# Kernel optimization log

Hardware: AMD Instinct MI355X
Metric: run time of the kernel (lower is better)

Reference implementation:

```python
import jax, jax.numpy as jnp
import numpy as np

N = 100000      # particles
E = 1600000     # particle pairs
B = 1024        # jets (batch); max(part_indicator)+1
C_IN = 64
HID = 32
T = 4           # n_terms
MID = 128
OUT = 128
EPS = 1e-5


def setup_inputs() -> dict:
    key = jax.random.key(0)
    ks = jax.random.split(key, 10)
    s = 0.05
    return {
        "part_features": jax.random.normal(ks[0], (N, C_IN), jnp.float32),
        "part_weight": jax.random.uniform(ks[1], (N, 1), jnp.float32),
        "pair_func": jax.random.normal(ks[2], (E, T), jnp.float32),
        "pair_head": jax.random.randint(ks[3], (E, 1), 0, N),
        "pair_tail": jax.random.randint(ks[4], (E, 1), 0, N),
        "part_indicator": jax.random.randint(ks[5], (N, 1), 0, B),
        "W_sc": jax.random.normal(ks[6], (OUT, C_IN), jnp.float32) * s,
        "g1": jnp.ones((C_IN,), jnp.float32), "b1": jnp.zeros((C_IN,), jnp.float32),
        "W1": jax.random.normal(ks[7], (HID, C_IN), jnp.float32) * s,
        "g2": jnp.ones((T * HID,), jnp.float32), "b2": jnp.zeros((T * HID,), jnp.float32),
        "W2": jax.random.normal(ks[8], (MID, T * HID), jnp.float32) * s,
        "g3": jnp.ones((MID,), jnp.float32), "b3": jnp.zeros((MID,), jnp.float32),
        "W3": jax.random.normal(ks[9], (OUT, MID), jnp.float32) * s,
    }


def weighted_bn(x, w, ind, gamma, beta):
    # segment-sum weighted features per jet -> batch stats over jets (training mode)
    jet = jax.ops.segment_sum(x * w, ind, num_segments=B)  # [B, C]
    mean = jet.mean(0)
    var = jet.var(0, ddof=1)  # unbiased, matches torch var(0, unbiased=True)
    return (x - mean) / jnp.sqrt(var + EPS) * gamma + beta


def reference(part_features, part_weight, pair_func, pair_head, pair_tail,
              part_indicator, W_sc, g1, b1, W1, g2, b2, W2, g3, b3, W3):
    ind = part_indicator[:, 0]
    head = pair_head[:, 0]
    tail = pair_tail[:, 0]

    short_cut = part_features @ W_sc.T                       # [N, OUT]

    h = jax.nn.relu(weighted_bn(part_features, part_weight, ind, g1, b1))
    h = h @ W1.T                                             # [N, HID]
    h = h * part_weight

    # gather tail features, expand by polynomial terms, scatter-add to head
    msg = (h[tail][:, :, None] * pair_func[:, None, :T]).reshape(E, HID * T)
    agg = jax.ops.segment_sum(msg, head, num_segments=N)     # [N, HID*T]

    h = jax.nn.relu(weighted_bn(agg, part_weight, ind, g2, b2)) @ W2.T  # [N, MID]
    h = jax.nn.relu(weighted_bn(h, part_weight, ind, g3, b3)) @ W3.T    # [N, OUT]
    return h + short_cut
```

## Files before the change

kernel.cpp:

```cpp
#include <hip/hip_runtime.h>

#define N_NODES 100000
#define N_EDGES 1600000
#define NB      1024
#define EPSF    1e-5f

#define SCHUNK 256
#define SNBLK ((N_NODES + SCHUNK - 1) / SCHUNK)

#define BUK_SH  7
#define NBUK    ((N_NODES + 127) >> 7)
#define EPB     6400
#define NBA     ((N_EDGES + EPB - 1) / EPB)
#define NCB     (NBUK * NBA)
#define SNB2    ((NCB + SCHUNK - 1) / SCHUNK)
#define CAP     3072

typedef float f32x4  __attribute__((ext_vector_type(4)));
typedef short bf16x8 __attribute__((ext_vector_type(8)));

__device__ __forceinline__ float bf2f(unsigned short u) {
    union { unsigned int i; float f; } v; v.i = ((unsigned int)u) << 16; return v.f;
}
__device__ __forceinline__ unsigned short f2bf(float f) {
    union { float ff; unsigned int i; } v; v.ff = f;
    unsigned int r = v.i + 0x7FFFu + ((v.i >> 16) & 1u);
    return (unsigned short)(r >> 16);
}

template<int C>
__global__ __launch_bounds__(256) void stats_kernel(const float* __restrict__ jet,
                                                    const float* __restrict__ g,
                                                    const float* __restrict__ b,
                                                    float* __restrict__ scale,
                                                    float* __restrict__ shift) {
    int c = blockIdx.x;
    int t = threadIdx.x;
    float s = 0.f, s2 = 0.f;
    for (int r = t; r < NB; r += 256) {
        float v = jet[r * C + c];
        s += v; s2 += v * v;
    }
    __shared__ float ls[256], ls2[256];
    ls[t] = s; ls2[t] = s2;
    __syncthreads();
    for (int ofs = 128; ofs > 0; ofs >>= 1) {
        if (t < ofs) { ls[t] += ls[t + ofs]; ls2[t] += ls2[t + ofs]; }
        __syncthreads();
    }
    if (t == 0) {
        float mean = ls[0] / (float)NB;
        float var  = (ls2[0] - (float)NB * mean * mean) / (float)(NB - 1);
        float sc   = g[c] / sqrtf(var + EPSF);
        scale[c] = sc;
        shift[c] = b[c] - mean * sc;
    }
}

__global__ __launch_bounds__(256) void countI_kernel(const int* __restrict__ ind,
                                                     int* __restrict__ cntI) {
    int n = blockIdx.x * 256 + threadIdx.x;
    if (n < N_NODES) atomicAdd(&cntI[ind[n]], 1);
}

__global__ __launch_bounds__(256) void count_head_kernel(const int* __restrict__ head,
                                                         int* __restrict__ cnt) {
    int e = blockIdx.x * 256 + threadIdx.x;
    if (e < N_EDGES) atomicAdd(&cnt[head[e]], 1);
}

__global__ __launch_bounds__(1024) void countCB_kernel(const int* __restrict__ head,
                                                       int* __restrict__ cnt_cb) {
    __shared__ int h[NBUK];
    int tid = threadIdx.x;
    int blk = blockIdx.x;
    for (int i = tid; i < NBUK; i += 1024) h[i] = 0;
    __syncthreads();
    int e0 = blk * EPB;
    for (int k = tid; k < EPB; k += 1024) {
        int e = e0 + k;
        if (e < N_EDGES) atomicAdd(&h[head[e] >> BUK_SH], 1);
    }
    __syncthreads();
    for (int i = tid; i < NBUK; i += 1024) cnt_cb[i * NBA + blk] = h[i];
}

__global__ __launch_bounds__(SCHUNK) void scanA_kernel(const int* __restrict__ cnt,
                                                       int* __restrict__ part, int n) {
    __shared__ int ls[SCHUNK];
    int t = threadIdx.x;
    int i = blockIdx.x * SCHUNK + t;
    ls[t] = (i < n) ? cnt[i] : 0;
    __syncthreads();
    for (int ofs = SCHUNK / 2; ofs > 0; ofs >>= 1) {
        if (t < ofs) ls[t] += ls[t + ofs];
        __syncthreads();
    }
    if (t == 0) part[blockIdx.x] = ls[0];
}

__global__ __launch_bounds__(1024) void scanB_kernel(const int* __restrict__ in,
                                                     int* __restrict__ out,
                                                     int* __restrict__ out2, int n) {
    __shared__ int ls[1024];
    int t = threadIdx.x;
    int v = (t < n) ? in[t] : 0;
    ls[t] = v;
    __syncthreads();
    for (int ofs = 1; ofs < 1024; ofs <<= 1) {
        int u = (t >= ofs) ? ls[t - ofs] : 0;
        __syncthreads();
        ls[t] += u;
        __syncthreads();
    }
    if (t < n) {
        int e = ls[t] - v;
        out[t] = e;
        if (out2) out2[t] = e;
    }
}

__global__ __launch_bounds__(SCHUNK) void scanC_kernel(const int* __restrict__ cnt,
                                                       const int* __restrict__ poff,
                                                       int* __restrict__ base,
                                                       int* __restrict__ cursor, int n) {
    __shared__ int ls[SCHUNK];
    int t = threadIdx.x;
    int i = blockIdx.x * SCHUNK + t;
    int v = (i < n) ? cnt[i] : 0;
    ls[t] = v;
    __syncthreads();
    for (int ofs = 1; ofs < SCHUNK; ofs <<= 1) {
        int u = (t >= ofs) ? ls[t - ofs] : 0;
        __syncthreads();
        ls[t] += u;
        __syncthreads();
    }
    if (i < n) {
        int bse = poff[blockIdx.x] + ls[t] - v;
        base[i] = bse;
        cursor[i] = bse;
    }
}

__global__ __launch_bounds__(1024) void binC16_kernel(const int* __restrict__ head,
                                                      const int* __restrict__ tail,
                                                      const float* __restrict__ pf,
                                                      const int* __restrict__ cbase,
                                                      uint4* __restrict__ hb16) {
    __shared__ int cur[NBUK];
    int tid = threadIdx.x;
    int blk = blockIdx.x;
    for (int i = tid; i < NBUK; i += 1024) cur[i] = cbase[i * NBA + blk];
    __syncthreads();
    int e0 = blk * EPB;
    for (int k = tid; k < EPB; k += 1024) {
        int e = e0 + k;
        if (e < N_EDGES) {
            int hd = head[e];
            int b = hd >> BUK_SH;
            int slot = atomicAdd(&cur[b], 1);
            float4 pv = ((const float4*)pf)[e];
            uint4 rec;
            rec.x = (unsigned)tail[e] | ((unsigned)(hd & 127) << 21);
            rec.y = (unsigned)f2bf(pv.x) | ((unsigned)f2bf(pv.y) << 16);
            rec.z = (unsigned)f2bf(pv.z) | ((unsigned)f2bf(pv.w) << 16);
            rec.w = 0u;
            hb16[slot] = rec;
        }
    }
}

__global__ __launch_bounds__(512) void sortGather_kernel(const int* __restrict__ cbase,
                                                         const uint4* __restrict__ hb16,
                                                         const unsigned short* __restrict__ hs,
                                                         unsigned short* __restrict__ agg) {
    __shared__ int hcnt[128];
    __shared__ int hbase[128];
    __shared__ int hcur[128];
    __shared__ int tail_l[CAP];
    __shared__ unsigned pf_l[2 * CAP];
    int tid = threadIdx.x;
    int b = blockIdx.x;
    int lo = cbase[b * NBA];
    int hi = (b + 1 < NBUK) ? cbase[(b + 1) * NBA] : N_EDGES;
    int cnt = hi - lo;
    if (tid < 128) hcnt[tid] = 0;
    __syncthreads();

    int wv = tid >> 6, lane = tid & 63;
    int i = lane >> 1, half = lane & 1;

    if (cnt <= CAP) {
        uint4 r0, r1, r2, r3, r4, r5;
        int k0 = lo + tid;
        bool v0 = (k0 < hi),            v1 = (k0 + 512 < hi);
        bool v2 = (k0 + 1024 < hi),     v3 = (k0 + 1536 < hi);
        bool v4 = (k0 + 2048 < hi),     v5 = (k0 + 2560 < hi);
        if (v0) r0 = hb16[k0];
        if (v1) r1 = hb16[k0 + 512];
        if (v2) r2 = hb16[k0 + 1024];
        if (v3) r3 = hb16[k0 + 1536];
        if (v4) r4 = hb16[k0 + 2048];
        if (v5) r5 = hb16[k0 + 2560];
        if (v0) atomicAdd(&hcnt[r0.x >> 21], 1);
        if (v1) atomicAdd(&hcnt[r1.x >> 21], 1);
        if (v2) atomicAdd(&hcnt[r2.x >> 21], 1);
        if (v3) atomicAdd(&hcnt[r3.x >> 21], 1);
        if (v4) atomicAdd(&hcnt[r4.x >> 21], 1);
        if (v5) atomicAdd(&hcnt[r5.x >> 21], 1);
        __syncthreads();
        if (tid < 128) hbase[tid] = hcnt[tid];
        __syncthreads();
        for (int ofs = 1; ofs < 128; ofs <<= 1) {
            int v = (tid < 128 && tid >= ofs) ? hbase[tid - ofs] : 0;
            __syncthreads();
            if (tid < 128) hbase[tid] += v;
            __syncthreads();
        }
        if (tid < 128) {
            int bse = hbase[tid] - hcnt[tid];
            hbase[tid] = bse;
            hcur[tid] = bse;
        }
        __syncthreads();
        if (v0) { int s = atomicAdd(&hcur[r0.x >> 21], 1); tail_l[s] = (int)(r0.x & 0xFFFFFu); pf_l[2*s] = r0.y; pf_l[2*s+1] = r0.z; }
        if (v1) { int s = atomicAdd(&hcur[r1.x >> 21], 1); tail_l[s] = (int)(r1.x & 0xFFFFFu); pf_l[2*s] = r1.y; pf_l[2*s+1] = r1.z; }
        if (v2) { int s = atomicAdd(&hcur[r2.x >> 21], 1); tail_l[s] = (int)(r2.x & 0xFFFFFu); pf_l[2*s] = r2.y; pf_l[2*s+1] = r2.z; }
        if (v3) { int s = atomicAdd(&hcur[r3.x >> 21], 1); tail_l[s] = (int)(r3.x & 0xFFFFFu); pf_l[2*s] = r3.y; pf_l[2*s+1] = r3.z; }
        if (v4) { int s = atomicAdd(&hcur[r4.x >> 21], 1); tail_l[s] = (int)(r4.x & 0xFFFFFu); pf_l[2*s] = r4.y; pf_l[2*s+1] = r4.z; }
        if (v5) { int s = atomicAdd(&hcur[r5.x >> 21], 1); tail_l[s] = (int)(r5.x & 0xFFFFFu); pf_l[2*s] = r5.y; pf_l[2*s+1] = r5.z; }
        __syncthreads();
        for (int j = 0; j < 16; j++) {
            int h7 = (wv << 4) + j;
            int n = (b << BUK_SH) + h7;
            if (n >= N_NODES) break;
            int s0 = hbase[h7], c = hcnt[h7];
            float a0 = 0.f, a1 = 0.f;
            int k = 0;
            for (; k + 4 <= c; k += 4) {
                int t0 = tail_l[s0 + k],     t1 = tail_l[s0 + k + 1];
                int t2 = tail_l[s0 + k + 2], t3 = tail_l[s0 + k + 3];
                unsigned u0 = pf_l[2 * (s0 + k) + half];
                unsigned u1 = pf_l[2 * (s0 + k + 1) + half];
                unsigned u2 = pf_l[2 * (s0 + k + 2) + half];
                unsigned u3 = pf_l[2 * (s0 + k + 3) + half];
                float h0 = bf2f(hs[(size_t)t0 * 32 + i]);
                float h1 = bf2f(hs[(size_t)t1 * 32 + i]);
                float h2 = bf2f(hs[(size_t)t2 * 32 + i]);
                float h3 = bf2f(hs[(size_t)t3 * 32 + i]);
                a0 += h0 * bf2f((unsigned short)(u0 & 0xFFFFu));
                a1 += h0 * bf2f((unsigned short)(u0 >> 16));
                a0 += h1 * bf2f((unsigned short)(u1 & 0xFFFFu));
                a1 += h1 * bf2f((unsigned short)(u1 >> 16));
                a0 += h2 * bf2f((unsigned short)(u2 & 0xFFFFu));
                a1 += h2 * bf2f((unsigned short)(u2 >> 16));
                a0 += h3 * bf2f((unsigned short)(u3 & 0xFFFFu));
                a1 += h3 * bf2f((unsigned short)(u3 >> 16));
            }
            for (; k < c; k++) {
                int t0 = tail_l[s0 + k];
                unsigned u0 = pf_l[2 * (s0 + k) + half];
                float h0 = bf2f(hs[(size_t)t0 * 32 + i]);
                a0 += h0 * bf2f((unsigned short)(u0 & 0xFFFFu));
                a1 += h0 * bf2f((unsigned short)(u0 >> 16));
            }
            unsigned pk = (unsigned)f2bf(a0) | ((unsigned)f2bf(a1) << 16);
            ((unsigned*)agg)[(size_t)n * 64 + lane] = pk;
        }
    } else {
        for (int j = 0; j < 16; j++) {
            int h7 = (wv << 4) + j;
            int n = (b << BUK_SH) + h7;
            if (n >= N_NODES) break;
            unsigned my = (unsigned)h7;
            float a0 = 0.f, a1 = 0.f;
            for (int k = lo; k < hi; k++) {
                uint4 rec = hb16[k];
                if ((rec.x >> 21) == my) {
                    unsigned u0 = (half == 0) ? rec.y : rec.z;
                    float h0 = bf2f(hs[(size_t)(rec.x & 0xFFFFFu) * 32 + i]);
                    a0 += h0 * bf2f((unsigned short)(u0 & 0xFFFFu));
                    a1 += h0 * bf2f((unsigned short)(u0 >> 16));
                }
            }
            unsigned pk = (unsigned)f2bf(a0) | ((unsigned)f2bf(a1) << 16);
            ((unsigned*)agg)[(size_t)n * 64 + lane] = pk;
        }
    }
}

__global__ __launch_bounds__(256) void escatterE_kernel(const int* __restrict__ head,
                                                        int* __restrict__ cursor,
                                                        int* __restrict__ eid) {
    int e = blockIdx.x * 256 + threadIdx.x;
    if (e >= N_EDGES) return;
    int slot = atomicAdd(&cursor[head[e]], 1);
    eid[slot] = e;
}

__global__ __launch_bounds__(256) void scatterI_kernel(const int* __restrict__ ind,
                                                       int* __restrict__ cursorI,
                                                       int* __restrict__ order) {
    int n = blockIdx.x * 256 + threadIdx.x;
    if (n < N_NODES) {
        int pos = atomicAdd(&cursorI[ind[n]], 1);
        order[pos] = n;
    }
}

template<int C>
__global__ __launch_bounds__(256) void bucket_jet_kernel(const float* __restrict__ xx,
                                                         const float* __restrict__ w,
                                                         const int* __restrict__ order,
                                                         const int* __restrict__ baseI,
                                                         const int* __restrict__ cntI,
                                                         float* __restrict__ jet) {
    constexpr int G = 256 / C;
    __shared__ float red[256];
    int b = blockIdx.x;
    int g = threadIdx.x / C;
    int c = threadIdx.x % C;
    int s0 = baseI[b], m = cntI[b];
    float s = 0.f;
    for (int k = g; k < m; k += G) {
        int n = order[s0 + k];
        s += xx[(size_t)n * C + c] * w[n];
    }
    red[threadIdx.x] = s;
    __syncthreads();
    for (int half = G / 2; half > 0; half >>= 1) {
        if (g < half) red[g * C + c] += red[(g + half) * C + c];
        __syncthreads();
    }
    if (g == 0) jet[b * C + c] = red[c];
}

__global__ __launch_bounds__(256) void bucket_jet_bf128_kernel(const unsigned short* __restrict__ xx,
                                                               const float* __restrict__ w,
                                                               const int* __restrict__ order,
                                                               const int* __restrict__ baseI,
                                                               const int* __restrict__ cntI,
                                                               float* __restrict__ jet) {
    __shared__ float redA[256], redB[256];
    int b = blockIdx.x;
    int g  = threadIdx.x >> 6;
    int c2 = threadIdx.x & 63;
    int s0 = baseI[b], m = cntI[b];
    float a0 = 0.f, a1 = 0.f;
    for (int k = g; k < m; k += 4) {
        int n = order[s0 + k];
        float wn = w[n];
        unsigned u = ((const unsigned*)xx)[(size_t)n * 64 + c2];
        a0 += bf2f((unsigned short)(u & 0xFFFFu)) * wn;
        a1 += bf2f((unsigned short)(u >> 16)) * wn;
    }
    redA[threadIdx.x] = a0; redB[threadIdx.x] = a1;
    __syncthreads();
    for (int half = 2; half > 0; half >>= 1) {
        if (g < half) {
            redA[g * 64 + c2] += redA[(g + half) * 64 + c2];
            redB[g * 64 + c2] += redB[(g + half) * 64 + c2];
        }
        __syncthreads();
    }
    if (g == 0) {
        jet[b * 128 + 2 * c2]     = redA[c2];
        jet[b * 128 + 2 * c2 + 1] = redB[c2];
    }
}

#define TILE1 64
__global__ __launch_bounds__(256) void fused1_kernel(const float* __restrict__ x,
                                                     const float* __restrict__ w,
                                                     const float* __restrict__ scale,
                                                     const float* __restrict__ shift,
                                                     const float* __restrict__ W1,
                                                     unsigned short* __restrict__ hs) {
    __shared__ __align__(16) unsigned short xnb[TILE1 * 64];
    __shared__ __align__(16) unsigned short w1b[32 * 64];
    int tid = threadIdx.x;
    int n0  = blockIdx.x * TILE1;
    char* xnb_ = (char*)xnb; char* w1b_ = (char*)w1b;

    for (int idx = tid; idx < TILE1 * 8; idx += 256) {
        int r = idx >> 3, c0 = (idx & 7) << 3;
        int n = n0 + r;
        float4 vA = make_float4(0.f, 0.f, 0.f, 0.f), vB = vA;
        if (n < N_NODES) {
            vA = *(const float4*)&x[(size_t)n * 64 + c0];
            vB = *(const float4*)&x[(size_t)n * 64 + c0 + 4];
        }
        float4 scA = *(const float4*)&scale[c0], scB = *(const float4*)&scale[c0 + 4];
        float4 shA = *(const float4*)&shift[c0], shB = *(const float4*)&shift[c0 + 4];
        unsigned short na[8];
        na[0] = f2bf(fmaxf(fmaf(vA.x, scA.x, shA.x), 0.f));
        na[1] = f2bf(fmaxf(fmaf(vA.y, scA.y, shA.y), 0.f));
        na[2] = f2bf(fmaxf(fmaf(vA.z, scA.z, shA.z), 0.f));
        na[3] = f2bf(fmaxf(fmaf(vA.w, scA.w, shA.w), 0.f));
        na[4] = f2bf(fmaxf(fmaf(vB.x, scB.x, shB.x), 0.f));
        na[5] = f2bf(fmaxf(fmaf(vB.y, scB.y, shB.y), 0.f));
        na[6] = f2bf(fmaxf(fmaf(vB.z, scB.z, shB.z), 0.f));
        na[7] = f2bf(fmaxf(fmaf(vB.w, scB.w, shB.w), 0.f));
        int byte = ((r << 7) + ((idx & 7) << 4)) ^ ((r & 7) << 4);
        *(bf16x8*)(xnb_ + byte) = *(bf16x8*)na;
    }
    for (int idx = tid; idx < 32 * 8; idx += 256) {
        int r = idx >> 3, c0 = (idx & 7) << 3;
        float4 vA = *(const float4*)&W1[(size_t)r * 64 + c0];
        float4 vB = *(const float4*)&W1[(size_t)r * 64 + c0 + 4];
        unsigned short ua[8];
        ua[0] = f2bf(vA.x); ua[1] = f2bf(vA.y); ua[2] = f2bf(vA.z); ua[3] = f2bf(vA.w);
        ua[4] = f2bf(vB.x); ua[5] = f2bf(vB.y); ua[6] = f2bf(vB.z); ua[7] = f2bf(vB.w);
        int byte = ((r << 7) + ((idx & 7) << 4)) ^ ((r & 7) << 4);
        *(bf16x8*)(w1b_ + byte) = *(bf16x8*)ua;
    }
    __syncthreads();

    int wv   = tid >> 6;
    int lane = tid & 63;
    int l15  = lane & 15;
    int lhi  = lane >> 4;

    f32x4 acc[2];
    acc[0] = (f32x4){0.f, 0.f, 0.f, 0.f};
    acc[1] = (f32x4){0.f, 0.f, 0.f, 0.f};

#pragma unroll
    for (int ks = 0; ks < 2; ks++) {
        int rA = (wv << 4) + l15;
        int byteA = ((rA << 7) + (ks << 6) + (lhi << 4)) ^ ((rA & 7) << 4);
        bf16x8 a = *(const bf16x8*)(xnb_ + byteA);
#pragma unroll
        for (int cf = 0; cf < 2; cf++) {
            int rB = (cf << 4) + l15;
            int byteB = ((rB << 7) + (ks << 6) + (lhi << 4)) ^ ((rB & 7) << 4);
            bf16x8 b = *(const bf16x8*)(w1b_ + byteB);
            acc[cf] = __builtin_amdgcn_mfma_f32_16x16x32_bf16(a, b, acc[cf], 0, 0, 0);
        }
    }

#pragma unroll
    for (int cf = 0; cf < 2; cf++) {
        int co = (cf << 4) + l15;
#pragma unroll
        for (int j = 0; j < 4; j++) {
            int n = n0 + (wv << 4) + (lhi << 2) + j;
            if (n < N_NODES) hs[(size_t)n * 32 + co] = f2bf(acc[cf][j] * w[n]);
        }
    }
}

__global__ __launch_bounds__(256) void gather2_kernel(const int* __restrict__ base,
                                                      const int* __restrict__ cnt,
                                                      const int* __restrict__ eid,
                                                      const int* __restrict__ tail,
                                                      const float* __restrict__ pf,
                                                      const unsigned short* __restrict__ hs,
                                                      unsigned short* __restrict__ agg) {
    int n = blockIdx.x * 4 + (threadIdx.x >> 6);
    if (n >= N_NODES) return;
    int lane = threadIdx.x & 63;
    int i = lane >> 1;
    int half = lane & 1;
    int s0 = base[n], c = cnt[n];
    float a0 = 0.f, a1 = 0.f;
    for (int k = 0; k < c; k++) {
        int e0 = eid[s0 + k];
        int t0 = tail[e0];
        float2 p0 = *(const float2*)&pf[(size_t)e0 * 4 + half * 2];
        float h0 = bf2f(hs[(size_t)t0 * 32 + i]);
        a0 += h0 * p0.x; a1 += h0 * p0.y;
    }
    unsigned pk = (unsigned)f2bf(a0) | ((unsigned)f2bf(a1) << 16);
    ((unsigned*)agg)[(size_t)n * 64 + lane] = pk;
}

__global__ __launch_bounds__(256) void edge_kernel(const int* __restrict__ head,
                                                   const int* __restrict__ tail,
                                                   const float* __restrict__ pf,
                                                   const unsigned short* __restrict__ hs,
                                                   float* __restrict__ agg) {
    long long tid = (long long)blockIdx.x * 256 + threadIdx.x;
    if (tid >= (long long)N_EDGES * 128) return;
    int e = (int)(tid >> 7);
    int j = (int)(tid & 127);
    int i = j >> 2, t = j & 3;
    float v = bf2f(hs[(size_t)tail[e] * 32 + i]) * pf[(size_t)e * 4 + t];
    atomicAdd(&agg[(size_t)head[e] * 128 + j], v);
}

#define TILE2 64
template<int INBF, int OUTBF>
__global__ __launch_bounds__(256) void fused2_kernel(const void* __restrict__ xin_,
                                                     const float* __restrict__ scale,
                                                     const float* __restrict__ shift,
                                                     const float* __restrict__ W,
                                                     void* __restrict__ yout_) {
    __shared__ __align__(16) unsigned short xnb[TILE2 * 128];
    __shared__ __align__(16) unsigned short wb[128 * 128];
    int tid = threadIdx.x;
    int n0  = blockIdx.x * TILE2;
    char* xbase = (char*)xnb;
    char* wbase = (char*)wb;

    for (int idx = tid; idx < TILE2 * 16; idx += 256) {
        int r = idx >> 4;
        int c0 = (idx & 15) << 3;
        int n = n0 + r;
        float f[8];
        if (n < N_NODES) {
            if (INBF) {
                const unsigned short* xu = (const unsigned short*)xin_;
                uint4 U = *(const uint4*)(xu + (size_t)n * 128 + c0);
                f[0] = bf2f((unsigned short)(U.x & 0xFFFFu)); f[1] = bf2f((unsigned short)(U.x >> 16));
                f[2] = bf2f((unsigned short)(U.y & 0xFFFFu)); f[3] = bf2f((unsigned short)(U.y >> 16));
                f[4] = bf2f((unsigned short)(U.z & 0xFFFFu)); f[5] = bf2f((unsigned short)(U.z >> 16));
                f[6] = bf2f((unsigned short)(U.w & 0xFFFFu)); f[7] = bf2f((unsigned short)(U.w >> 16));
            } else {
                const float* xf = (const float*)xin_;
                float4 vA = *(const float4*)&xf[(size_t)n * 128 + c0];
                float4 vB = *(const float4*)&xf[(size_t)n * 128 + c0 + 4];
                f[0] = vA.x; f[1] = vA.y; f[2] = vA.z; f[3] = vA.w;
                f[4] = vB.x; f[5] = vB.y; f[6] = vB.z; f[7] = vB.w;
            }
        } else {
#pragma unroll
            for (int q = 0; q < 8; q++) f[q] = 0.f;
        }
        unsigned short ua[8];
#pragma unroll
        for (int q = 0; q < 8; q++)
            ua[q] = f2bf(fmaxf(fmaf(f[q], scale[c0 + q], shift[c0 + q]), 0.f));
        int byte = ((r << 8) + ((idx & 15) << 4)) ^ ((r & 7) << 4);
        *(bf16x8*)(xbase + byte) = *(bf16x8*)ua;
    }
    for (int idx = tid; idx < 128 * 16; idx += 256) {
        int r = idx >> 4;
        int c0 = (idx & 15) << 3;
        float4 vA = *(const float4*)&W[(size_t)r * 128 + c0];
        float4 vB = *(const float4*)&W[(size_t)r * 128 + c0 + 4];
        unsigned short ua[8];
        ua[0] = f2bf(vA.x); ua[1] = f2bf(vA.y); ua[2] = f2bf(vA.z); ua[3] = f2bf(vA.w);
        ua[4] = f2bf(vB.x); ua[5] = f2bf(vB.y); ua[6] = f2bf(vB.z); ua[7] = f2bf(vB.w);
        int byte = ((r << 8) + ((idx & 15) << 4)) ^ ((r & 7) << 4);
        *(bf16x8*)(wbase + byte) = *(bf16x8*)ua;
    }
    __syncthreads();

    int wv   = tid >> 6;
    int lane = tid & 63;
    int l15  = lane & 15;
    int lhi  = lane >> 4;

    f32x4 acc[8];
#pragma unroll
    for (int cf = 0; cf < 8; cf++) acc[cf] = (f32x4){0.f, 0.f, 0.f, 0.f};

#pragma unroll
    for (int ks = 0; ks < 4; ks++) {
        int rA = (wv << 4) + l15;
        int byteA = ((rA << 8) + (ks << 6) + (lhi << 4)) ^ ((rA & 7) << 4);
        bf16x8 a = *(const bf16x8*)(xbase + byteA);
#pragma unroll
        for (int cf = 0; cf < 8; cf++) {
            int rB = (cf << 4) + l15;
            int byteB = ((rB << 8) + (ks << 6) + (lhi << 4)) ^ ((rB & 7) << 4);
            bf16x8 b = *(const bf16x8*)(wbase + byteB);
            acc[cf] = __builtin_amdgcn_mfma_f32_16x16x32_bf16(a, b, acc[cf], 0, 0, 0);
        }
    }

#pragma unroll
    for (int cf = 0; cf < 8; cf++) {
        int col = (cf << 4) + l15;
#pragma unroll
        for (int j = 0; j < 4; j++) {
            int n = n0 + (wv << 4) + (lhi << 2) + j;
            if (n < N_NODES) {
                float v = acc[cf][j];
                if (OUTBF) ((unsigned short*)yout_)[(size_t)n * 128 + col] = f2bf(v);
                else       ((float*)yout_)[(size_t)n * 128 + col] = v;
            }
        }
    }
}

template<int INBF>
__global__ __launch_bounds__(256) void fused3_kernel(const void* __restrict__ h2_,
                                                     const float* __restrict__ x,
                                                     const float* __restrict__ scale,
                                                     const float* __restrict__ shift,
                                                     const float* __restrict__ Wsc,
                                                     const float* __restrict__ W3,
                                                     float* __restrict__ out) {
    __shared__ __align__(16) unsigned short xnb[TILE2 * 128];
    __shared__ __align__(16) unsigned short xrb[TILE2 * 64];
    __shared__ __align__(16) unsigned short wb[128 * 128];
    int tid = threadIdx.x;
    int n0  = blockIdx.x * TILE2;
    char* xbase = (char*)xnb;
    char* rbase = (char*)xrb;
    char* wbase = (char*)wb;

    for (int idx = tid; idx < TILE2 * 16; idx += 256) {
        int r = idx >> 4;
        int c0 = (idx & 15) << 3;
        int n = n0 + r;
        float f[8];
        if (n < N_NODES) {
            if (INBF) {
                const unsigned short* xu = (const unsigned short*)h2_;
                uint4 U = *(const uint4*)(xu + (size_t)n * 128 + c0);
                f[0] = bf2f((unsigned short)(U.x & 0xFFFFu)); f[1] = bf2f((unsigned short)(U.x >> 16));
                f[2] = bf2f((unsigned short)(U.y & 0xFFFFu)); f[3] = bf2f((unsigned short)(U.y >> 16));
                f[4] = bf2f((unsigned short)(U.z & 0xFFFFu)); f[5] = bf2f((unsigned short)(U.z >> 16));
                f[6] = bf2f((unsigned short)(U.w & 0xFFFFu)); f[7] = bf2f((unsigned short)(U.w >> 16));
            } else {
                const float* xf = (const float*)h2_;
                float4 vA = *(const float4*)&xf[(size_t)n * 128 + c0];
                float4 vB = *(const float4*)&xf[(size_t)n * 128 + c0 + 4];
                f[0] = vA.x; f[1] = vA.y; f[2] = vA.z; f[3] = vA.w;
                f[4] = vB.x; f[5] = vB.y; f[6] = vB.z; f[7] = vB.w;
            }
        } else {
#pragma unroll
            for (int q = 0; q < 8; q++) f[q] = 0.f;
        }
        unsigned short ua[8];
#pragma unroll
        for (int q = 0; q < 8; q++)
            ua[q] = f2bf(fmaxf(fmaf(f[q], scale[c0 + q], shift[c0 + q]), 0.f));
        int byte = ((r << 8) + ((idx & 15) << 4)) ^ ((r & 7) << 4);
        *(bf16x8*)(xbase + byte) = *(bf16x8*)ua;
    }
    for (int idx = tid; idx < TILE2 * 8; idx += 256) {
        int r = idx >> 3, c0 = (idx & 7) << 3;
        int n = n0 + r;
        float4 vA = make_float4(0.f, 0.f, 0.f, 0.f), vB = vA;
        if (n < N_NODES) {
            vA = *(const float4*)&x[(size_t)n * 64 + c0];
            vB = *(const float4*)&x[(size_t)n * 64 + c0 + 4];
        }
        unsigned short ua[8];
        ua[0] = f2bf(vA.x); ua[1] = f2bf(vA.y); ua[2] = f2bf(vA.z); ua[3] = f2bf(vA.w);
        ua[4] = f2bf(vB.x); ua[5] = f2bf(vB.y); ua[6] = f2bf(vB.z); ua[7] = f2bf(vB.w);
        int byte = ((r << 7) + ((idx & 7) << 4)) ^ ((r & 7) << 4);
        *(bf16x8*)(rbase + byte) = *(bf16x8*)ua;
    }
    for (int idx = tid; idx < 128 * 8; idx += 256) {
        int r = idx >> 3, c0 = (idx & 7) << 3;
        float4 vA = *(const float4*)&Wsc[(size_t)r * 64 + c0];
        float4 vB = *(const float4*)&Wsc[(size_t)r * 64 + c0 + 4];
        unsigned short ua[8];
        ua[0] = f2bf(vA.x); ua[1] = f2bf(vA.y); ua[2] = f2bf(vA.z); ua[3] = f2bf(vA.w);
        ua[4] = f2bf(vB.x); ua[5] = f2bf(vB.y); ua[6] = f2bf(vB.z); ua[7] = f2bf(vB.w);
        int byte = ((r << 7) + ((idx & 7) << 4)) ^ ((r & 7) << 4);
        *(bf16x8*)(wbase + byte) = *(bf16x8*)ua;
    }
    __syncthreads();

    int wv   = tid >> 6;
    int lane = tid & 63;
    int l15  = lane & 15;
    int lhi  = lane >> 4;

    f32x4 acc[8];
#pragma unroll
    for (int cf = 0; cf < 8; cf++) acc[cf] = (f32x4){0.f, 0.f, 0.f, 0.f};

#pragma unroll
    for (int ks = 0; ks < 2; ks++) {
        int rA = (wv << 4) + l15;
        int byteA = ((rA << 7) + (ks << 6) + (lhi << 4)) ^ ((rA & 7) << 4);
        bf16x8 a = *(const bf16x8*)(rbase + byteA);
#pragma unroll
        for (int cf = 0; cf < 8; cf++) {
            int rB = (cf << 4) + l15;
            int byteB = ((rB << 7) + (ks << 6) + (lhi << 4)) ^ ((rB & 7) << 4);
            bf16x8 b = *(const bf16x8*)(wbase + byteB);
            acc[cf] = __builtin_amdgcn_mfma_f32_16x16x32_bf16(a, b, acc[cf], 0, 0, 0);
        }
    }
    __syncthreads();
    for (int idx = tid; idx < 128 * 16; idx += 256) {
        int r = idx >> 4;
        int c0 = (idx & 15) << 3;
        float4 vA = *(const float4*)&W3[(size_t)r * 128 + c0];
        float4 vB = *(const float4*)&W3[(size_t)r * 128 + c0 + 4];
        unsigned short ua[8];
        ua[0] = f2bf(vA.x); ua[1] = f2bf(vA.y); ua[2] = f2bf(vA.z); ua[3] = f2bf(vA.w);
        ua[4] = f2bf(vB.x); ua[5] = f2bf(vB.y); ua[6] = f2bf(vB.z); ua[7] = f2bf(vB.w);
        int byte = ((r << 8) + ((idx & 15) << 4)) ^ ((r & 7) << 4);
        *(bf16x8*)(wbase + byte) = *(bf16x8*)ua;
    }
    __syncthreads();

#pragma unroll
    for (int ks = 0; ks < 4; ks++) {
        int rA = (wv << 4) + l15;
        int byteA = ((rA << 8) + (ks << 6) + (lhi << 4)) ^ ((rA & 7) << 4);
        bf16x8 a = *(const bf16x8*)(xbase + byteA);
#pragma unroll
        for (int cf = 0; cf < 8; cf++) {
            int rB = (cf << 4) + l15;
            int byteB = ((rB << 8) + (ks << 6) + (lhi << 4)) ^ ((rB & 7) << 4);
            bf16x8 b = *(const bf16x8*)(wbase + byteB);
            acc[cf] = __builtin_amdgcn_mfma_f32_16x16x32_bf16(a, b, acc[cf], 0, 0, 0);
        }
    }

#pragma unroll
    for (int cf = 0; cf < 8; cf++) {
        int col = (cf << 4) + l15;
#pragma unroll
        for (int j = 0; j < 4; j++) {
            int n = n0 + (wv << 4) + (lhi << 2) + j;
            if (n < N_NODES) out[(size_t)n * 128 + col] = acc[cf][j];
        }
    }
}

extern "C" void kernel_launch(void* const* d_in, const int* in_sizes, int n_in,
                              void* d_out, int out_size, void* d_ws, size_t ws_size,
                              hipStream_t stream) {
    const float* x    = (const float*)d_in[0];
    const float* w    = (const float*)d_in[1];
    const float* pf   = (const float*)d_in[2];
    const int*   head = (const int*)d_in[3];
    const int*   tail = (const int*)d_in[4];
    const int*   ind  = (const int*)d_in[5];
    const float* Wsc  = (const float*)d_in[6];
    const float* g1   = (const float*)d_in[7];
    const float* b1   = (const float*)d_in[8];
    const float* W1   = (const float*)d_in[9];
    const float* g2   = (const float*)d_in[10];
    const float* b2   = (const float*)d_in[11];
    const float* W2   = (const float*)d_in[12];
    const float* g3   = (const float*)d_in[13];
    const float* b3   = (const float*)d_in[14];
    const float* W3   = (const float*)d_in[15];
    float* out = (float*)d_out;

    char* p = (char*)d_ws;
    unsigned short* hs = (unsigned short*)p;  p += (size_t)N_NODES * 32 * 2;
    char* aggraw = p;                         p += (size_t)N_NODES * 128 * 4;
    unsigned short* agg_bf = (unsigned short*)aggraw;
    float*          agg_f  = (float*)aggraw;
    uint4* hb16 = (uint4*)(aggraw + (size_t)N_NODES * 128 * 2);
    float* jet1 = (float*)p;                  p += 1024 * 64 * 4;
    float* jet2 = (float*)p;                  p += 1024 * 128 * 4;
    float* jet3 = (float*)p;                  p += 1024 * 128 * 4;
    float* sc1 = (float*)p; p += 64 * 4;  float* sh1 = (float*)p; p += 64 * 4;
    float* sc2 = (float*)p; p += 128 * 4; float* sh2 = (float*)p; p += 128 * 4;
    float* sc3 = (float*)p; p += 128 * 4; float* sh3 = (float*)p; p += 128 * 4;
    int* cnt_e    = (int*)p; p += (size_t)N_NODES * 4;
    int* base_e   = (int*)p; p += (size_t)N_NODES * 4;
    int* cursor_e = (int*)p; p += (size_t)N_NODES * 4;
    int* part     = (int*)p; p += 1024 * 4;
    int* cntI     = (int*)p; p += 1024 * 4;
    int* baseI    = (int*)p; p += 1024 * 4;
    int* cursorI  = (int*)p; p += 1024 * 4;
    int* order    = (int*)p; p += (size_t)N_NODES * 4;
    int* eid      = (int*)p; p += (size_t)N_EDGES * 4;
    size_t need_t2 = (size_t)(p - (char*)d_ws);
    int* cnt_cb   = (int*)p; p += (size_t)NCB * 4;
    int* cbase    = (int*)p; p += (size_t)NCB * 4;
    int* ccur     = (int*)p; p += (size_t)NCB * 4;
    size_t need_t1 = (size_t)(p - (char*)d_ws);
    int tier = (ws_size >= need_t1) ? 1 : (ws_size >= need_t2) ? 2 : 3;

    hipMemsetAsync(cntI, 0, 1024 * sizeof(int), stream);
    countI_kernel<<<(N_NODES + 255) / 256, 256, 0, stream>>>(ind, cntI);
    scanB_kernel<<<1, 1024, 0, stream>>>(cntI, baseI, cursorI, 1024);
    scatterI_kernel<<<(N_NODES + 255) / 256, 256, 0, stream>>>(ind, cursorI, order);

    bucket_jet_kernel<64><<<1024, 256, 0, stream>>>(x, w, order, baseI, cntI, jet1);
    stats_kernel<64><<<64, 256, 0, stream>>>(jet1, g1, b1, sc1, sh1);

    fused1_kernel<<<(N_NODES + TILE1 - 1) / TILE1, 256, 0, stream>>>(
        x, w, sc1, sh1, W1, hs);

    if (tier == 1) {
        countCB_kernel<<<NBA, 1024, 0, stream>>>(head, cnt_cb);
        scanA_kernel<<<SNB2, SCHUNK, 0, stream>>>(cnt_cb, part, NCB);
        scanB_kernel<<<1, 1024, 0, stream>>>(part, part, nullptr, SNB2);
        scanC_kernel<<<SNB2, SCHUNK, 0, stream>>>(cnt_cb, part, cbase, ccur, NCB);
        binC16_kernel<<<NBA, 1024, 0, stream>>>(head, tail, pf, cbase, hb16);
        sortGather_kernel<<<NBUK, 512, 0, stream>>>(cbase, hb16, hs, agg_bf);
    } else if (tier == 2) {
        hipMemsetAsync(cnt_e, 0, N_NODES * sizeof(int), stream);
        count_head_kernel<<<(N_EDGES + 255) / 256, 256, 0, stream>>>(head, cnt_e);
        scanA_kernel<<<SNBLK, SCHUNK, 0, stream>>>(cnt_e, part, N_NODES);
        scanB_kernel<<<1, 1024, 0, stream>>>(part, part, nullptr, SNBLK);
        scanC_kernel<<<SNBLK, SCHUNK, 0, stream>>>(cnt_e, part, base_e, cursor_e, N_NODES);
        escatterE_kernel<<<(N_EDGES + 255) / 256, 256, 0, stream>>>(
            head, cursor_e, eid);
        gather2_kernel<<<(N_NODES + 3) / 4, 256, 0, stream>>>(
            base_e, cnt_e, eid, tail, pf, hs, agg_bf);
    }

    if (tier <= 2) {
        bucket_jet_bf128_kernel<<<1024, 256, 0, stream>>>(agg_bf, w, order, baseI, cntI, jet2);
        stats_kernel<128><<<128, 256, 0, stream>>>(jet2, g2, b2, sc2, sh2);
        fused2_kernel<1, 1><<<(N_NODES + TILE2 - 1) / TILE2, 256, 0, stream>>>(
            agg_bf, sc2, sh2, W2, agg_bf);
        bucket_jet_bf128_kernel<<<1024, 256, 0, stream>>>(agg_bf, w, order, baseI, cntI, jet3);
        stats_kernel<128><<<128, 256, 0, stream>>>(jet3, g3, b3, sc3, sh3);
        fused3_kernel<1><<<(N_NODES + TILE2 - 1) / TILE2, 256, 0, stream>>>(
            agg_bf, x, sc3, sh3, Wsc, W3, out);
    } else {
        hipMemsetAsync(agg_f, 0, (size_t)N_NODES * 128 * sizeof(float), stream);
        edge_kernel<<<(int)(((long long)N_EDGES * 128) / 256), 256, 0, stream>>>(
            head, tail, pf, hs, agg_f);
        bucket_jet_kernel<128><<<1024, 256, 0, stream>>>(agg_f, w, order, baseI, cntI, jet2);
        stats_kernel<128><<<128, 256, 0, stream>>>(jet2, g2, b2, sc2, sh2);
        fused2_kernel<0, 0><<<(N_NODES + TILE2 - 1) / TILE2, 256, 0, stream>>>(
            agg_f, sc2, sh2, W2, agg_f);
        bucket_jet_kernel<128><<<1024, 256, 0, stream>>>(agg_f, w, order, baseI, cntI, jet3);
        stats_kernel<128><<<128, 256, 0, stream>>>(jet3, g3, b3, sc3, sh3);
        fused3_kernel<0><<<(N_NODES + TILE2 - 1) / TILE2, 256, 0, stream>>>(
            agg_f, x, sc3, sh3, Wsc, W3, out);
    }

    (void)in_sizes; (void)n_in; (void)out_size;
}
```

Measured before the change: 282.4 us.

## Replace per-chunk bucket scan with global bucket counts and atomic slot reservation

The edge binning no longer writes a bucket-by-chunk count matrix and runs a three-pass scan over it. Each block now adds its bucket counts atomically into a small global array, which a single-block scan turns into bucket offsets. The binning kernel recounts its chunk locally and reserves contiguous ranges with global atomics. This removes two scan launches and the large count matrix, but edge order within a bucket becomes nondeterministic and head indices are read one extra time. The gather loop is also unrolled from 4 to 8 edges to put more independent loads in flight.

New measurement: 291.3 us. 3.2% more time.

```diff
diff --git a/kernel.cpp b/kernel.cpp
--- a/kernel.cpp
+++ b/kernel.cpp
@@ -12,8 +12,6 @@
 #define NBUK    ((N_NODES + 127) >> 7)
 #define EPB     6400
 #define NBA     ((N_EDGES + EPB - 1) / EPB)
-#define NCB     (NBUK * NBA)
-#define SNB2    ((NCB + SCHUNK - 1) / SCHUNK)
 #define CAP     3072
 
 typedef float f32x4  __attribute__((ext_vector_type(4)));
@@ -69,8 +67,8 @@
     if (e < N_EDGES) atomicAdd(&cnt[head[e]], 1);
 }
 
-__global__ __launch_bounds__(1024) void countCB_kernel(const int* __restrict__ head,
-                                                       int* __restrict__ cnt_cb) {
+__global__ __launch_bounds__(1024) void countB2_kernel(const int* __restrict__ head,
+                                                       int* __restrict__ bcnt) {
     __shared__ int h[NBUK];
     int tid = threadIdx.x;
     int blk = blockIdx.x;
@@ -82,7 +80,8 @@
         if (e < N_EDGES) atomicAdd(&h[head[e] >> BUK_SH], 1);
     }
     __syncthreads();
-    for (int i = tid; i < NBUK; i += 1024) cnt_cb[i * NBA + blk] = h[i];
+    for (int i = tid; i < NBUK; i += 1024)
+        if (h[i] > 0) atomicAdd(&bcnt[i], h[i]);
 }
 
 __global__ __launch_bounds__(SCHUNK) void scanA_kernel(const int* __restrict__ cnt,
@@ -143,23 +142,32 @@
     }
 }
 
-__global__ __launch_bounds__(1024) void binC16_kernel(const int* __restrict__ head,
-                                                      const int* __restrict__ tail,
-                                                      const float* __restrict__ pf,
-                                                      const int* __restrict__ cbase,
-                                                      uint4* __restrict__ hb16) {
-    __shared__ int cur[NBUK];
+__global__ __launch_bounds__(1024) void binC16b_kernel(const int* __restrict__ head,
+                                                       const int* __restrict__ tail,
+                                                       const float* __restrict__ pf,
+                                                       int* __restrict__ bcur,
+                                                       uint4* __restrict__ hb16) {
+    __shared__ int lcnt[NBUK];
+    __shared__ int lcur[NBUK];
     int tid = threadIdx.x;
     int blk = blockIdx.x;
-    for (int i = tid; i < NBUK; i += 1024) cur[i] = cbase[i * NBA + blk];
+    for (int i = tid; i < NBUK; i += 1024) lcnt[i] = 0;
     __syncthreads();
     int e0 = blk * EPB;
+    for (int k = tid; k < EPB; k += 1024) {
+        int e = e0 + k;
+        if (e < N_EDGES) atomicAdd(&lcnt[head[e] >> BUK_SH], 1);
+    }
+    __syncthreads();
+    for (int i = tid; i < NBUK; i += 1024)
+        lcur[i] = (lcnt[i] > 0) ? atomicAdd(&bcur[i], lcnt[i]) : 0;
+    __syncthreads();
     for (int k = tid; k < EPB; k += 1024) {
         int e = e0 + k;
         if (e < N_EDGES) {
             int hd = head[e];
             int b = hd >> BUK_SH;
-            int slot = atomicAdd(&cur[b], 1);
+            int slot = atomicAdd(&lcur[b], 1);
             float4 pv = ((const float4*)pf)[e];
             uint4 rec;
             rec.x = (unsigned)tail[e] | ((unsigned)(hd & 127) << 21);
@@ -171,7 +179,8 @@
     }
 }
 
-__global__ __launch_bounds__(512) void sortGather_kernel(const int* __restrict__ cbase,
+__global__ __launch_bounds__(512) void sortGather_kernel(const int* __restrict__ bbase,
+                                                         const int* __restrict__ bcnt,
                                                          const uint4* __restrict__ hb16,
                                                          const unsigned short* __restrict__ hs,
                                                          unsigned short* __restrict__ agg) {
@@ -182,9 +191,9 @@
     __shared__ unsigned pf_l[2 * CAP];
     int tid = threadIdx.x;
     int b = blockIdx.x;
-    int lo = cbase[b * NBA];
-    int hi = (b + 1 < NBUK) ? cbase[(b + 1) * NBA] : N_EDGES;
-    int cnt = hi - lo;
+    int lo = bbase[b];
+    int cnt = bcnt[b];
+    int hi = lo + cnt;
     if (tid < 128) hcnt[tid] = 0;
     __syncthreads();
 
@@ -238,17 +247,23 @@
             int s0 = hbase[h7], c = hcnt[h7];
             float a0 = 0.f, a1 = 0.f;
             int k = 0;
-            for (; k + 4 <= c; k += 4) {
-                int t0 = tail_l[s0 + k],     t1 = tail_l[s0 + k + 1];
-                int t2 = tail_l[s0 + k + 2], t3 = tail_l[s0 + k + 3];
-                unsigned u0 = pf_l[2 * (s0 + k) + half];
-                unsigned u1 = pf_l[2 * (s0 + k + 1) + half];
-                unsigned u2 = pf_l[2 * (s0 + k + 2) + half];
-                unsigned u3 = pf_l[2 * (s0 + k + 3) + half];
+            for (; k + 8 <= c; k += 8) {
+                int t0 = tail_l[s0+k],   t1 = tail_l[s0+k+1];
+                int t2 = tail_l[s0+k+2], t3 = tail_l[s0+k+3];
+                int t4 = tail_l[s0+k+4], t5 = tail_l[s0+k+5];
+                int t6 = tail_l[s0+k+6], t7 = tail_l[s0+k+7];
                 float h0 = bf2f(hs[(size_t)t0 * 32 + i]);
                 float h1 = bf2f(hs[(size_t)t1 * 32 + i]);
                 float h2 = bf2f(hs[(size_t)t2 * 32 + i]);
                 float h3 = bf2f(hs[(size_t)t3 * 32 + i]);
+                float h4 = bf2f(hs[(size_t)t4 * 32 + i]);
+                float h5 = bf2f(hs[(size_t)t5 * 32 + i]);
+                float h6 = bf2f(hs[(size_t)t6 * 32 + i]);
+                float h7f = bf2f(hs[(size_t)t7 * 32 + i]);
+                unsigned u0 = pf_l[2*(s0+k)+half],   u1 = pf_l[2*(s0+k+1)+half];
+                unsigned u2 = pf_l[2*(s0+k+2)+half], u3 = pf_l[2*(s0+k+3)+half];
+                unsigned u4 = pf_l[2*(s0+k+4)+half], u5 = pf_l[2*(s0+k+5)+half];
+                unsigned u6 = pf_l[2*(s0+k+6)+half], u7 = pf_l[2*(s0+k+7)+half];
                 a0 += h0 * bf2f((unsigned short)(u0 & 0xFFFFu));
                 a1 += h0 * bf2f((unsigned short)(u0 >> 16));
                 a0 += h1 * bf2f((unsigned short)(u1 & 0xFFFFu));
@@ -257,6 +272,14 @@
                 a1 += h2 * bf2f((unsigned short)(u2 >> 16));
                 a0 += h3 * bf2f((unsigned short)(u3 & 0xFFFFu));
                 a1 += h3 * bf2f((unsigned short)(u3 >> 16));
+                a0 += h4 * bf2f((unsigned short)(u4 & 0xFFFFu));
+                a1 += h4 * bf2f((unsigned short)(u4 >> 16));
+                a0 += h5 * bf2f((unsigned short)(u5 & 0xFFFFu));
+                a1 += h5 * bf2f((unsigned short)(u5 >> 16));
+                a0 += h6 * bf2f((unsigned short)(u6 & 0xFFFFu));
+                a1 += h6 * bf2f((unsigned short)(u6 >> 16));
+                a0 += h7f * bf2f((unsigned short)(u7 & 0xFFFFu));
+                a1 += h7f * bf2f((unsigned short)(u7 >> 16));
             }
             for (; k < c; k++) {
                 int t0 = tail_l[s0 + k];
@@ -764,9 +787,9 @@
     int* order    = (int*)p; p += (size_t)N_NODES * 4;
     int* eid      = (int*)p; p += (size_t)N_EDGES * 4;
     size_t need_t2 = (size_t)(p - (char*)d_ws);
-    int* cnt_cb   = (int*)p; p += (size_t)NCB * 4;
-    int* cbase    = (int*)p; p += (size_t)NCB * 4;
-    int* ccur     = (int*)p; p += (size_t)NCB * 4;
+    int* bcnt  = (int*)p; p += NBUK * 4;
+    int* bbase = (int*)p; p += NBUK * 4;
+    int* bcur  = (int*)p; p += NBUK * 4;
     size_t need_t1 = (size_t)(p - (char*)d_ws);
     int tier = (ws_size >= need_t1) ? 1 : (ws_size >= need_t2) ? 2 : 3;
 
@@ -782,12 +805,11 @@
         x, w, sc1, sh1, W1, hs);
 
     if (tier == 1) {
-        countCB_kernel<<<NBA, 1024, 0, stream>>>(head, cnt_cb);
-        scanA_kernel<<<SNB2, SCHUNK, 0, stream>>>(cnt_cb, part, NCB);
-        scanB_kernel<<<1, 1024, 0, stream>>>(part, part, nullptr, SNB2);
-        scanC_kernel<<<SNB2, SCHUNK, 0, stream>>>(cnt_cb, part, cbase, ccur, NCB);
-        binC16_kernel<<<NBA, 1024, 0, stream>>>(head, tail, pf, cbase, hb16);
-        sortGather_kernel<<<NBUK, 512, 0, stream>>>(cbase, hb16, hs, agg_bf);
+        hipMemsetAsync(bcnt, 0, NBUK * sizeof(int), stream);
+        countB2_kernel<<<NBA, 1024, 0, stream>>>(head, bcnt);
+        scanB_kernel<<<1, 1024, 0, stream>>>(bcnt, bbase, bcur, NBUK);
+        binC16b_kernel<<<NBA, 1024, 0, stream>>>(head, tail, pf, bcur, hb16);
+        sortGather_kernel<<<NBUK, 512, 0, stream>>>(bbase, bcnt, hb16, hs, agg_bf);
     } else if (tier == 2) {
         hipMemsetAsync(cnt_e, 0, N_NODES * sizeof(int), stream);
         count_head_kernel<<<(N_EDGES + 255) / 256, 256, 0, stream>>>(head, cnt_e);
```
